# Optimization experiments

Hardware: AMD Instinct MI355X
Metric: run time of the kernel (lower is better)

The kernel has to match this reference:

```python
import jax, jax.numpy as jnp
import numpy as np

B, T, D = 2, 2048, 2048
H, KV = 16, 4
HD = D // H           # head_dim = 128
G = H // KV           # group size = 4
VOCAB = 32000


def setup_inputs() -> dict:
    key = jax.random.key(0)
    k1, k2, k3, k4, k5, k6 = jax.random.split(key, 6)
    hidden_state = jax.random.normal(k1, (B, T, D), dtype=jnp.float32)
    ids = jax.random.randint(k2, (B, T), 1, VOCAB)  # avoid pad id 0
    ids = ids.at[:, T - T // 8:].set(0)             # trailing padding
    inputs_id = ids.astype(jnp.int64)
    s = 1.0 / np.sqrt(D)
    Wq = jax.random.normal(k3, (D, H * HD), dtype=jnp.float32) * s
    Wk = jax.random.normal(k4, (D, KV * HD), dtype=jnp.float32) * s
    Wv = jax.random.normal(k5, (D, KV * HD), dtype=jnp.float32) * s
    Wo = jax.random.normal(k6, (H * HD, D), dtype=jnp.float32) * s
    return {"hidden_state": hidden_state, "inputs_id": inputs_id,
            "Wq": Wq, "Wk": Wk, "Wv": Wv, "Wo": Wo}


def reference(hidden_state, inputs_id, Wq, Wk, Wv, Wo):
    b, t = inputs_id.shape
    # masks: padding over KEYS, combined with causal
    pad = (inputs_id != 0)[:, None, None, :]                 # [B,1,1,T]
    causal = jnp.tril(jnp.ones((t, t), dtype=bool))[None, None]  # [1,1,T,T]
    mask = pad & causal                                       # [B,1,T,T]

    q = (hidden_state @ Wq).reshape(b, t, H, HD).transpose(0, 2, 1, 3)  # [B,H,T,hd]
    k = (hidden_state @ Wk).reshape(b, t, KV, HD)
    v = (hidden_state @ Wv).reshape(b, t, KV, HD)
    # faithful to torch expand/reshape: head h -> kv head (h % KV)
    k = jnp.broadcast_to(k[:, :, None], (b, t, G, KV, HD)).reshape(b, t, H, HD).transpose(0, 2, 1, 3)
    v = jnp.broadcast_to(v[:, :, None], (b, t, G, KV, HD)).reshape(b, t, H, HD).transpose(0, 2, 1, 3)

    scores = jnp.einsum('bhqd,bhkd->bhqk', q, k) / np.sqrt(HD)
    scores = jnp.where(mask, scores, -jnp.inf)
    probs = jax.nn.softmax(scores, axis=-1)
    out = jnp.einsum('bhqk,bhkd->bhqd', probs, v)             # [B,H,T,hd]
    out = out.transpose(0, 2, 1, 3).reshape(b, t, H * HD)
    return out @ Wo
```

## Files before the change

kernel.cpp:

```cpp
#include <hip/hip_runtime.h>

#define B_ 2
#define T_ 2048
#define D_ 2048
#define H_ 16
#define KV_ 4
#define HD_ 128
#define M_ (B_*T_)

typedef __attribute__((ext_vector_type(8))) short s8v;
typedef __attribute__((ext_vector_type(4))) float f4v;
typedef __attribute__((ext_vector_type(16))) float f16v;
typedef __attribute__((ext_vector_type(8))) __bf16 b8v;
typedef __attribute__((ext_vector_type(4))) unsigned u4v;

__device__ __forceinline__ short f2bs(float f) {
  unsigned u = __builtin_bit_cast(unsigned, f);
  u += 0x7fffu + ((u >> 16) & 1u);
  return (short)(u >> 16);
}
__device__ __forceinline__ void plswap2(unsigned &x, unsigned &y) {
  asm volatile("v_permlane32_swap_b32 %0, %1" : "+v"(x), "+v"(y));
}
__device__ __forceinline__ unsigned cvtpk(float lo, float hi) {
  unsigned r;
  asm("v_cvt_pk_bf16_f32 %0, %1, %2" : "=v"(r) : "v"(lo), "v"(hi));
  return r;
}

__global__ void cast_bf16_kernel(const float* __restrict__ in, short* __restrict__ out, int n4) {
  int i = blockIdx.x * 256 + threadIdx.x;
  if (i >= n4) return;
  float4 v = reinterpret_cast<const float4*>(in)[i];
  short4 o;
  o.x = f2bs(v.x); o.y = f2bs(v.y); o.z = f2bs(v.z); o.w = f2bs(v.w);
  reinterpret_cast<short4*>(out)[i] = o;
}

__global__ void tcast_all_kernel(const float* __restrict__ Wq, const float* __restrict__ Wk,
                                 const float* __restrict__ Wv, const float* __restrict__ Wo,
                                 short* __restrict__ WT, short* __restrict__ WoT) {
  __shared__ float t[32][33];
  int bid = blockIdx.x;
  const float* W; short* dst; int N, rowoff;
  if (bid < 4096)      { W = Wq; dst = WT;  N = 2048; rowoff = 0;    }
  else if (bid < 5120) { W = Wk; dst = WT;  N = 512;  rowoff = 2048; bid -= 4096; }
  else if (bid < 6144) { W = Wv; dst = WT;  N = 512;  rowoff = 2560; bid -= 5120; }
  else                 { W = Wo; dst = WoT; N = 2048; rowoff = 0;    bid -= 6144; }
  const int nbl = N >> 5;
  const int nb = (bid % nbl) * 32, kb = (bid / nbl) * 32;
  const int tx = threadIdx.x, ty = threadIdx.y;
#pragma unroll
  for (int j = 0; j < 4; ++j)
    t[ty + j*8][tx] = W[(size_t)(kb + ty + j*8) * N + nb + tx];
  __syncthreads();
#pragma unroll
  for (int j = 0; j < 4; ++j)
    dst[(size_t)(rowoff + nb + ty + j*8) * 2048 + kb + tx] = f2bs(t[tx][ty + j*8]);
}

template<int MODE>
__global__ __launch_bounds__(256) void gemm_bt_kernel(const short* __restrict__ A,
                                                      const short* __restrict__ BT,
                                                      void* __restrict__ Cv,
                                                      short* __restrict__ Kv,
                                                      short* __restrict__ Vt,
                                                      int M, int N, int K) {
  __shared__ alignas(16) short As[2][128*32];
  __shared__ alignas(16) short Bs[2][128*32];
  const int tid  = threadIdx.x;
  const int wave = tid >> 6;
  const int lane = tid & 63;
  const int lr = lane & 15;
  const int lk = (lane >> 4) * 8;
  const int m0 = blockIdx.y * 128;
  const int n0 = blockIdx.x * 128;
  const int wr = (wave >> 1) * 64;
  const int wc = (wave & 1) * 64;

  const int srow = tid >> 2, skc = tid & 3;
  const short* gaBase = A  + (size_t)(m0 + srow) * K + skc*8;
  const short* gbBase = BT + (size_t)(n0 + srow) * K + skc*8;
  const short* gaBase2 = A  + (size_t)(m0 + 64 + srow) * K + skc*8;
  const short* gbBase2 = BT + (size_t)(n0 + 64 + srow) * K + skc*8;
  const int ldsOff  = (wave*64) * 8;
  const int ldsOff2 = (256 + wave*64) * 8;

  f4v acc[4][4];
#pragma unroll
  for (int m = 0; m < 4; ++m)
#pragma unroll
    for (int n = 0; n < 4; ++n) acc[m][n] = (f4v)0.0f;

  {
    __builtin_amdgcn_global_load_lds((const __attribute__((address_space(1))) void*)gaBase,
        (__attribute__((address_space(3))) void*)(&As[0][0] + ldsOff), 16, 0, 0);
    __builtin_amdgcn_global_load_lds((const __attribute__((address_space(1))) void*)gbBase,
        (__attribute__((address_space(3))) void*)(&Bs[0][0] + ldsOff), 16, 0, 0);
    __builtin_amdgcn_global_load_lds((const __attribute__((address_space(1))) void*)gaBase2,
        (__attribute__((address_space(3))) void*)(&As[0][0] + ldsOff2), 16, 0, 0);
    __builtin_amdgcn_global_load_lds((const __attribute__((address_space(1))) void*)gbBase2,
        (__attribute__((address_space(3))) void*)(&Bs[0][0] + ldsOff2), 16, 0, 0);
  }

  int cur = 0;
  for (int k0 = 0; k0 < K; k0 += 32) {
    __syncthreads();
    if (k0 + 32 < K) {
      const int kn = k0 + 32;
      short* a1 = &As[cur^1][0];
      short* b1 = &Bs[cur^1][0];
      __builtin_amdgcn_global_load_lds((const __attribute__((address_space(1))) void*)(gaBase + kn),
          (__attribute__((address_space(3))) void*)(a1 + ldsOff), 16, 0, 0);
      __builtin_amdgcn_global_load_lds((const __attribute__((address_space(1))) void*)(gbBase + kn),
          (__attribute__((address_space(3))) void*)(b1 + ldsOff), 16, 0, 0);
      __builtin_amdgcn_global_load_lds((const __attribute__((address_space(1))) void*)(gaBase2 + kn),
          (__attribute__((address_space(3))) void*)(a1 + ldsOff2), 16, 0, 0);
      __builtin_amdgcn_global_load_lds((const __attribute__((address_space(1))) void*)(gbBase2 + kn),
          (__attribute__((address_space(3))) void*)(b1 + ldsOff2), 16, 0, 0);
    }
    const short* Ac = &As[cur][0];
    const short* Bc = &Bs[cur][0];
    s8v af[4], bfv[4];
#pragma unroll
    for (int m = 0; m < 4; ++m)
      af[m] = *reinterpret_cast<const s8v*>(Ac + (wr + m*16 + lr)*32 + lk);
#pragma unroll
    for (int n = 0; n < 4; ++n)
      bfv[n] = *reinterpret_cast<const s8v*>(Bc + (wc + n*16 + lr)*32 + lk);
#pragma unroll
    for (int m = 0; m < 4; ++m)
#pragma unroll
      for (int n = 0; n < 4; ++n)
        acc[m][n] = __builtin_amdgcn_mfma_f32_16x16x32_bf16(
            __builtin_bit_cast(b8v, af[m]), __builtin_bit_cast(b8v, bfv[n]),
            acc[m][n], 0, 0, 0);
    cur ^= 1;
  }

  if (MODE == 3 && n0 >= 2560) {
#pragma unroll
    for (int m = 0; m < 4; ++m) {
#pragma unroll
      for (int n = 0; n < 4; ++n) {
        const int col = n0 + wc + n*16 + lr - 2560;
        const int row = m0 + wr + m*16 + (lane >> 4)*4;
        short4 o;
        o.x = f2bs(acc[m][n][0]); o.y = f2bs(acc[m][n][1]);
        o.z = f2bs(acc[m][n][2]); o.w = f2bs(acc[m][n][3]);
        *reinterpret_cast<short4*>(Vt + (size_t)col * M + row) = o;
      }
    }
  } else {
#pragma unroll
    for (int m = 0; m < 4; ++m) {
#pragma unroll
      for (int n = 0; n < 4; ++n) {
#pragma unroll
        for (int i = 0; i < 4; ++i) {
          const int row = m0 + wr + m*16 + (lane >> 4)*4 + i;
          const int col = n0 + wc + n*16 + lr;
          if (MODE == 1)
            reinterpret_cast<float*>(Cv)[(size_t)row * N + col] = acc[m][n][i];
          else if (col < 2048)
            reinterpret_cast<short*>(Cv)[(size_t)row * 2048 + col] = f2bs(acc[m][n][i]);
          else
            Kv[(size_t)row * 512 + (col - 2048)] = f2bs(acc[m][n][i]);
        }
      }
    }
  }
}

__device__ __forceinline__ void stage_tile(short* KsBuf, short* VtBuf,
                                           const short* __restrict__ Kb,
                                           const short* __restrict__ Vtg,
                                           int bT, int kv0, int kvh,
                                           int tid, int wave) {
#pragma unroll
  for (int j = 0; j < 4; ++j) {
    const int f = j*256 + tid;
    const int row = f >> 4, cd = f & 15, cs = cd ^ (row & 7);
    const short* g = Kb + (size_t)(bT + kv0 + row)*512 + kvh*HD_ + cs*8;
    short* l = KsBuf + (j*256 + wave*64) * 8;
    __builtin_amdgcn_global_load_lds((const __attribute__((address_space(1))) void*)g,
                                     (__attribute__((address_space(3))) void*)l, 16, 0, 0);
  }
#pragma unroll
  for (int j = 0; j < 4; ++j) {
    const int f = j*256 + tid;
    const int d = f >> 3, cd = f & 7, cs = cd ^ (d & 7);
    const short* g = Vtg + (size_t)(kvh*HD_ + d)*M_ + bT + kv0 + cs*8;
    short* l = VtBuf + (j*256 + wave*64) * 8;
    __builtin_amdgcn_global_load_lds((const __attribute__((address_space(1))) void*)g,
                                     (__attribute__((address_space(3))) void*)l, 16, 0, 0);
  }
}

__global__ __launch_bounds__(256, 2) void attn_kernel(const short* __restrict__ Q,
                                                      const short* __restrict__ Kb,
                                                      const short* __restrict__ Vtg,
                                                      const int* __restrict__ ids,
                                                      short* __restrict__ AO) {
  __shared__ alignas(16) short Ks[2][64*128];
  __shared__ alignas(16) short Vt[2][128*64];

  const int bid = blockIdx.x;
  const int g   = bid & 31;
  const int gr  = bid >> 5;
  const int p   = (gr < 8) ? (15 - gr) : (gr - 8);
  const int h   = g & (H_-1);
  const int b   = g >> 4;
  const int kvh = h & (KV_-1);
  const int tid = threadIdx.x;
  const int wq  = tid >> 6;
  const int lane = tid & 63;
  const int ql  = lane & 31;
  const int hi  = lane >> 5;
  const int bT  = b * T_;
  const int q0  = p * 128;
  const int qrow = q0 + wq*32 + ql;
  const int nt  = 2*(p+1);
  const float SC = 0.08838834764831845f * 1.4426950408889634f;

  s8v qf[8];
  const size_t qgbase = (size_t)(bT + qrow) * (H_*HD_) + h*HD_;
#pragma unroll
  for (int mm = 0; mm < 8; ++mm)
    qf[mm] = *reinterpret_cast<const s8v*>(Q + qgbase + mm*16 + hi*8);

  f16v oacc[4];
#pragma unroll
  for (int n = 0; n < 4; ++n) oacc[n] = (f16v)0.0f;
  float m_run = -1.0e30f, lsum = 0.0f;

  stage_tile(Ks[0], Vt[0], Kb, Vtg, bT, 0, kvh, tid, wq);
  int cur = 0;
  for (int t = 0; t < nt; ++t) {
    __syncthreads();
    if (t + 1 < nt)
      stage_tile(Ks[cur^1], Vt[cur^1], Kb, Vtg, bT, (t+1)*64, kvh, tid, wq);
    const int kv0 = t * 64;
    const char* KsC = reinterpret_cast<const char*>(Ks[cur]);
    const char* VtC = reinterpret_cast<const char*>(Vt[cur]);

    const unsigned long long pmask = __ballot(ids[bT + kv0 + lane] != 0);

    f16v sacc[2];
    sacc[0] = (f16v)0.0f; sacc[1] = (f16v)0.0f;
#pragma unroll
    for (int mm = 0; mm < 8; ++mm) {
#pragma unroll
      for (int kb = 0; kb < 2; ++kb) {
        const int row = kb*32 + ql;
        s8v kf = *reinterpret_cast<const s8v*>(KsC +
            ((row*256 + mm*32 + hi*16) ^ ((row & 7) << 4)));
        sacc[kb] = __builtin_amdgcn_mfma_f32_32x32x16_bf16(
            __builtin_bit_cast(b8v, kf), __builtin_bit_cast(b8v, qf[mm]), sacc[kb], 0, 0, 0);
      }
    }

    float tm[16];
#pragma unroll
    for (int r = 0; r < 16; ++r) tm[r] = fmaxf(sacc[0][r], sacc[1][r]);
#pragma unroll
    for (int r = 0; r < 8; ++r) tm[r] = fmaxf(tm[r], tm[r+8]);
#pragma unroll
    for (int r = 0; r < 4; ++r) tm[r] = fmaxf(tm[r], tm[r+4]);
    tm[0] = fmaxf(fmaxf(tm[0], tm[1]), fmaxf(tm[2], tm[3]));
    const float mx = fmaxf(tm[0], __shfl_xor(tm[0], 32));

    if (!__all(mx <= m_run + 20.0f)) {
      const float mn = fmaxf(m_run, mx);
      const float corr = exp2f((m_run - mn) * SC);
      lsum *= corr;
#pragma unroll
      for (int n = 0; n < 4; ++n)
#pragma unroll
        for (int r = 0; r < 16; ++r) oacc[n][r] *= corr;
      m_run = mn;
    }
    const float nm = -m_run * SC;
    const bool fast = (kv0 + 63 <= q0 + wq*32) && (pmask == ~0ull);

    float psum = 0.0f;
#pragma unroll
    for (int kb = 0; kb < 2; ++kb) {
      float pv[16];
#pragma unroll
      for (int r = 0; r < 16; ++r)
        pv[r] = exp2f(fmaf(sacc[kb][r], SC, nm));
      if (!fast) {
        const int th = qrow - kv0 - kb*32 - 4*hi;
        const unsigned cw = (th >= 28) ? 0xffffffffu
                          : ((th < 0) ? 0u : ((2u << th) - 1u));
        const unsigned vm = cw & (unsigned)(pmask >> (kb*32 + 4*hi));
#pragma unroll
        for (int r = 0; r < 16; ++r) {
          const int C = (r & 3) + 8*(r >> 2);
          pv[r] = ((vm >> C) & 1u) ? pv[r] : 0.0f;
        }
      }
      float ps[8];
#pragma unroll
      for (int r = 0; r < 8; ++r) ps[r] = pv[r] + pv[r+8];
#pragma unroll
      for (int r = 0; r < 4; ++r) ps[r] += ps[r+4];
      psum += (ps[0] + ps[1]) + (ps[2] + ps[3]);

      unsigned pa = cvtpk(pv[0],  pv[1]),  pb = cvtpk(pv[2],  pv[3]);
      unsigned pc = cvtpk(pv[4],  pv[5]),  pd = cvtpk(pv[6],  pv[7]);
      unsigned pe = cvtpk(pv[8],  pv[9]),  pf_ = cvtpk(pv[10], pv[11]);
      unsigned pg = cvtpk(pv[12], pv[13]), ph = cvtpk(pv[14], pv[15]);
      plswap2(pa, pc);  plswap2(pb, pd);
      plswap2(pe, pg);  plswap2(pf_, ph);
      u4v pw0 = {pa, pb, pc, pd};
      u4v pw1 = {pe, pf_, pg, ph};

#pragma unroll
      for (int s = 0; s < 2; ++s) {
        const b8v pf = __builtin_bit_cast(b8v, s ? pw1 : pw0);
        const int ks = 2*kb + s;
#pragma unroll
        for (int n = 0; n < 4; ++n) {
          const int d = n*32 + ql;
          s8v vf = *reinterpret_cast<const s8v*>(VtC +
              ((d*128 + ks*32 + hi*16) ^ ((d & 7) << 4)));
          oacc[n] = __builtin_amdgcn_mfma_f32_32x32x16_bf16(
              __builtin_bit_cast(b8v, vf), pf, oacc[n], 0, 0, 0);
        }
      }
    }
    lsum += psum + __shfl_xor(psum, 32);
    cur ^= 1;
  }

  const float inv = 1.0f / fmaxf(lsum, 1.0e-37f);
  const size_t obase = (size_t)(bT + qrow) * (H_*HD_) + h*HD_;
#pragma unroll
  for (int n = 0; n < 4; ++n) {
#pragma unroll
    for (int j = 0; j < 4; ++j) {
      short4 o;
      o.x = f2bs(oacc[n][4*j+0] * inv);
      o.y = f2bs(oacc[n][4*j+1] * inv);
      o.z = f2bs(oacc[n][4*j+2] * inv);
      o.w = f2bs(oacc[n][4*j+3] * inv);
      *reinterpret_cast<short4*>(AO + obase + n*32 + 8*j + 4*hi) = o;
    }
  }
}

extern "C" void kernel_launch(void* const* d_in, const int* in_sizes, int n_in,
                              void* d_out, int out_size, void* d_ws, size_t ws_size,
                              hipStream_t stream) {
  const float* hs = (const float*)d_in[0];
  const int*  ids = (const int*)d_in[1];
  const float* Wq = (const float*)d_in[2];
  const float* Wk = (const float*)d_in[3];
  const float* Wv = (const float*)d_in[4];
  const float* Wo = (const float*)d_in[5];
  char* ws = (char*)d_ws;

  short* hsb = (short*)(ws);
  short* WT  = (short*)(ws + (16u << 20));
  short* WoT = (short*)(ws + (28u << 20));
  short* Qb  = (short*)(ws + (36u << 20));
  short* Kb  = (short*)(ws + (52u << 20));
  short* Vtg = (short*)(ws + (56u << 20));
  short* AO  = hsb;
  float* out = (float*)d_out;

  cast_bf16_kernel<<<dim3((M_*D_/4 + 255)/256), dim3(256), 0, stream>>>(hs, hsb, M_*D_/4);
  tcast_all_kernel<<<dim3(10240), dim3(32, 8), 0, stream>>>(Wq, Wk, Wv, Wo, WT, WoT);

  gemm_bt_kernel<3><<<dim3(3072/128, 4096/128), dim3(256), 0, stream>>>(
      hsb, WT, Qb, Kb, Vtg, 4096, 3072, 2048);

  attn_kernel<<<dim3(512), dim3(256), 0, stream>>>(Qb, Kb, Vtg, ids, AO);

  gemm_bt_kernel<1><<<dim3(2048/128, 4096/128), dim3(256), 0, stream>>>(
      AO, WoT, out, nullptr, nullptr, 4096, 2048, 2048);
}
```

Before: 211.7 us.

## Software-pipeline attention: overlap next-tile QK MFMA with softmax/PV, triple-buffer V

After: 228.3 us. 1.08x slower.

```diff
diff --git a/kernel.cpp b/kernel.cpp
--- a/kernel.cpp
+++ b/kernel.cpp
@@ -28,7 +28,15 @@
   return r;
 }
 
-__global__ void cast_bf16_kernel(const float* __restrict__ in, short* __restrict__ out, int n4) {
+__global__ void cast_bf16_kernel(const float* __restrict__ in, short* __restrict__ out, int n4,
+                                 const int* __restrict__ ids, unsigned long long* __restrict__ pmA) {
+  if (blockIdx.x == 0 && threadIdx.x < 64) {
+    const int bb = threadIdx.x >> 5, tt = threadIdx.x & 31;
+    const int* p = ids + bb*T_ + tt*64;
+    unsigned long long m = 0;
+    for (int k = 0; k < 64; ++k) m |= (unsigned long long)(p[k] != 0) << k;
+    pmA[threadIdx.x] = m;
+  }
   int i = blockIdx.x * 256 + threadIdx.x;
   if (i >= n4) return;
   float4 v = reinterpret_cast<const float4*>(in)[i];
@@ -172,38 +180,149 @@
   }
 }
 
-__device__ __forceinline__ void stage_tile(short* KsBuf, short* VtBuf,
-                                           const short* __restrict__ Kb,
-                                           const short* __restrict__ Vtg,
-                                           int bT, int kv0, int kvh,
-                                           int tid, int wave) {
+__device__ __forceinline__ void stage_K(short* dst, const short* __restrict__ Kb,
+                                        int bT, int kv0, int kvh, int tid, int wave) {
 #pragma unroll
   for (int j = 0; j < 4; ++j) {
     const int f = j*256 + tid;
     const int row = f >> 4, cd = f & 15, cs = cd ^ (row & 7);
     const short* g = Kb + (size_t)(bT + kv0 + row)*512 + kvh*HD_ + cs*8;
-    short* l = KsBuf + (j*256 + wave*64) * 8;
+    short* l = dst + (j*256 + wave*64) * 8;
     __builtin_amdgcn_global_load_lds((const __attribute__((address_space(1))) void*)g,
                                      (__attribute__((address_space(3))) void*)l, 16, 0, 0);
   }
+}
+__device__ __forceinline__ void stage_V(short* dst, const short* __restrict__ Vtg,
+                                        int bT, int kv0, int kvh, int tid, int wave) {
 #pragma unroll
   for (int j = 0; j < 4; ++j) {
     const int f = j*256 + tid;
     const int d = f >> 3, cd = f & 7, cs = cd ^ (d & 7);
     const short* g = Vtg + (size_t)(kvh*HD_ + d)*M_ + bT + kv0 + cs*8;
-    short* l = VtBuf + (j*256 + wave*64) * 8;
+    short* l = dst + (j*256 + wave*64) * 8;
     __builtin_amdgcn_global_load_lds((const __attribute__((address_space(1))) void*)g,
                                      (__attribute__((address_space(3))) void*)l, 16, 0, 0);
   }
+}
+
+__device__ __forceinline__ void qk_mfma(const char* KsC, const s8v (&qf)[8],
+                                        int ql, int hi, f16v (&sacc)[2]) {
+  sacc[0] = (f16v)0.0f; sacc[1] = (f16v)0.0f;
+#pragma unroll
+  for (int mm = 0; mm < 8; ++mm) {
+#pragma unroll
+    for (int kb = 0; kb < 2; ++kb) {
+      const int row = kb*32 + ql;
+      s8v kf = *reinterpret_cast<const s8v*>(KsC +
+          ((row*256 + mm*32 + hi*16) ^ ((row & 7) << 4)));
+      sacc[kb] = __builtin_amdgcn_mfma_f32_32x32x16_bf16(
+          __builtin_bit_cast(b8v, kf), __builtin_bit_cast(b8v, qf[mm]), sacc[kb], 0, 0, 0);
+    }
+  }
+}
+
+__device__ __forceinline__ void attn_iter(
+    int t, int nt, int q0, int wq, int ql, int hi, int qrow, int bT, int kvh, int tid,
+    const s8v (&qf)[8], f16v (&scur)[2], f16v (&snxt)[2],
+    const char* kr, short* kw, const char* vr, short* vw,
+    const short* __restrict__ Kb, const short* __restrict__ Vtg,
+    unsigned long long &pm_cur, const unsigned long long* __restrict__ pmA, int pmBase,
+    f16v (&oacc)[4], float &m_run, float &lsum, float SC)
+{
+  if (t + 1 < nt) { asm volatile("s_waitcnt vmcnt(4)" ::: "memory"); }
+  else            { asm volatile("s_waitcnt vmcnt(0)" ::: "memory"); }
+  __builtin_amdgcn_s_barrier();
+  __builtin_amdgcn_sched_barrier(0);
+
+  if (t + 2 < nt) stage_K(kw, Kb, bT, (t+2)*64, kvh, tid, wq);
+  if (t + 1 < nt) qk_mfma(kr, qf, ql, hi, snxt);
+  unsigned long long pm_next = (t + 1 < nt) ? pmA[pmBase + t + 1] : 0ull;
+
+  const int kv0 = t * 64;
+  float tm[16];
+#pragma unroll
+  for (int r = 0; r < 16; ++r) tm[r] = fmaxf(scur[0][r], scur[1][r]);
+#pragma unroll
+  for (int r = 0; r < 8; ++r) tm[r] = fmaxf(tm[r], tm[r+8]);
+#pragma unroll
+  for (int r = 0; r < 4; ++r) tm[r] = fmaxf(tm[r], tm[r+4]);
+  tm[0] = fmaxf(fmaxf(tm[0], tm[1]), fmaxf(tm[2], tm[3]));
+  const float mx = fmaxf(tm[0], __shfl_xor(tm[0], 32));
+
+  if (!__all(mx <= m_run + 20.0f)) {
+    const float mn = fmaxf(m_run, mx);
+    const float corr = exp2f((m_run - mn) * SC);
+    lsum *= corr;
+#pragma unroll
+    for (int n = 0; n < 4; ++n)
+#pragma unroll
+      for (int r = 0; r < 16; ++r) oacc[n][r] *= corr;
+    m_run = mn;
+  }
+  const float nm = -m_run * SC;
+  const bool fast = (kv0 + 63 <= q0 + wq*32) && (pm_cur == ~0ull);
+
+  float psum = 0.0f;
+#pragma unroll
+  for (int kb = 0; kb < 2; ++kb) {
+    float pv[16];
+#pragma unroll
+    for (int r = 0; r < 16; ++r)
+      pv[r] = exp2f(fmaf(scur[kb][r], SC, nm));
+    if (!fast) {
+      const int th = qrow - kv0 - kb*32 - 4*hi;
+      const unsigned cw = (th >= 28) ? 0xffffffffu
+                        : ((th < 0) ? 0u : ((2u << th) - 1u));
+      const unsigned vm = cw & (unsigned)(pm_cur >> (kb*32 + 4*hi));
+#pragma unroll
+      for (int r = 0; r < 16; ++r) {
+        const int C = (r & 3) + 8*(r >> 2);
+        pv[r] = ((vm >> C) & 1u) ? pv[r] : 0.0f;
+      }
+    }
+    float ps[8];
+#pragma unroll
+    for (int r = 0; r < 8; ++r) ps[r] = pv[r] + pv[r+8];
+#pragma unroll
+    for (int r = 0; r < 4; ++r) ps[r] += ps[r+4];
+    psum += (ps[0] + ps[1]) + (ps[2] + ps[3]);
+
+    unsigned pa = cvtpk(pv[0],  pv[1]),  pb = cvtpk(pv[2],  pv[3]);
+    unsigned pc = cvtpk(pv[4],  pv[5]),  pd = cvtpk(pv[6],  pv[7]);
+    unsigned pe = cvtpk(pv[8],  pv[9]),  pf_ = cvtpk(pv[10], pv[11]);
+    unsigned pg = cvtpk(pv[12], pv[13]), ph = cvtpk(pv[14], pv[15]);
+    plswap2(pa, pc);  plswap2(pb, pd);
+    plswap2(pe, pg);  plswap2(pf_, ph);
+    u4v pw0 = {pa, pb, pc, pd};
+    u4v pw1 = {pe, pf_, pg, ph};
+
+#pragma unroll
+    for (int s = 0; s < 2; ++s) {
+      const b8v pf = __builtin_bit_cast(b8v, s ? pw1 : pw0);
+      const int ks = 2*kb + s;
+#pragma unroll
+      for (int n = 0; n < 4; ++n) {
+        const int d = n*32 + ql;
+        s8v vf = *reinterpret_cast<const s8v*>(vr +
+            ((d*128 + ks*32 + hi*16) ^ ((d & 7) << 4)));
+        oacc[n] = __builtin_amdgcn_mfma_f32_32x32x16_bf16(
+            __builtin_bit_cast(b8v, vf), pf, oacc[n], 0, 0, 0);
+      }
+    }
+  }
+  lsum += psum + __shfl_xor(psum, 32);
+
+  if (t + 2 < nt) stage_V(vw, Vtg, bT, (t+2)*64, kvh, tid, wq);
+  pm_cur = pm_next;
 }
 
 __global__ __launch_bounds__(256, 2) void attn_kernel(const short* __restrict__ Q,
                                                       const short* __restrict__ Kb,
                                                       const short* __restrict__ Vtg,
-                                                      const int* __restrict__ ids,
+                                                      const unsigned long long* __restrict__ pmA,
                                                       short* __restrict__ AO) {
   __shared__ alignas(16) short Ks[2][64*128];
-  __shared__ alignas(16) short Vt[2][128*64];
+  __shared__ alignas(16) short Vs[3][128*64];
 
   const int bid = blockIdx.x;
   const int g   = bid & 31;
@@ -221,6 +340,7 @@
   const int q0  = p * 128;
   const int qrow = q0 + wq*32 + ql;
   const int nt  = 2*(p+1);
+  const int pmBase = b * 32;
   const float SC = 0.08838834764831845f * 1.4426950408889634f;
 
   s8v qf[8];
@@ -234,105 +354,28 @@
   for (int n = 0; n < 4; ++n) oacc[n] = (f16v)0.0f;
   float m_run = -1.0e30f, lsum = 0.0f;
 
-  stage_tile(Ks[0], Vt[0], Kb, Vtg, bT, 0, kvh, tid, wq);
-  int cur = 0;
-  for (int t = 0; t < nt; ++t) {
-    __syncthreads();
-    if (t + 1 < nt)
-      stage_tile(Ks[cur^1], Vt[cur^1], Kb, Vtg, bT, (t+1)*64, kvh, tid, wq);
-    const int kv0 = t * 64;
-    const char* KsC = reinterpret_cast<const char*>(Ks[cur]);
-    const char* VtC = reinterpret_cast<const char*>(Vt[cur]);
-
-    const unsigned long long pmask = __ballot(ids[bT + kv0 + lane] != 0);
-
-    f16v sacc[2];
-    sacc[0] = (f16v)0.0f; sacc[1] = (f16v)0.0f;
-#pragma unroll
-    for (int mm = 0; mm < 8; ++mm) {
-#pragma unroll
-      for (int kb = 0; kb < 2; ++kb) {
-        const int row = kb*32 + ql;
-        s8v kf = *reinterpret_cast<const s8v*>(KsC +
-            ((row*256 + mm*32 + hi*16) ^ ((row & 7) << 4)));
-        sacc[kb] = __builtin_amdgcn_mfma_f32_32x32x16_bf16(
-            __builtin_bit_cast(b8v, kf), __builtin_bit_cast(b8v, qf[mm]), sacc[kb], 0, 0, 0);
-      }
-    }
-
-    float tm[16];
-#pragma unroll
-    for (int r = 0; r < 16; ++r) tm[r] = fmaxf(sacc[0][r], sacc[1][r]);
-#pragma unroll
-    for (int r = 0; r < 8; ++r) tm[r] = fmaxf(tm[r], tm[r+8]);
-#pragma unroll
-    for (int r = 0; r < 4; ++r) tm[r] = fmaxf(tm[r], tm[r+4]);
-    tm[0] = fmaxf(fmaxf(tm[0], tm[1]), fmaxf(tm[2], tm[3]));
-    const float mx = fmaxf(tm[0], __shfl_xor(tm[0], 32));
-
-    if (!__all(mx <= m_run + 20.0f)) {
-      const float mn = fmaxf(m_run, mx);
-      const float corr = exp2f((m_run - mn) * SC);
-      lsum *= corr;
-#pragma unroll
-      for (int n = 0; n < 4; ++n)
-#pragma unroll
-        for (int r = 0; r < 16; ++r) oacc[n][r] *= corr;
-      m_run = mn;
-    }
-    const float nm = -m_run * SC;
-    const bool fast = (kv0 + 63 <= q0 + wq*32) && (pmask == ~0ull);
-
-    float psum = 0.0f;
-#pragma unroll
-    for (int kb = 0; kb < 2; ++kb) {
-      float pv[16];
-#pragma unroll
-      for (int r = 0; r < 16; ++r)
-        pv[r] = exp2f(fmaf(sacc[kb][r], SC, nm));
-      if (!fast) {
-        const int th = qrow - kv0 - kb*32 - 4*hi;
-        const unsigned cw = (th >= 28) ? 0xffffffffu
-                          : ((th < 0) ? 0u : ((2u << th) - 1u));
-        const unsigned vm = cw & (unsigned)(pmask >> (kb*32 + 4*hi));
-#pragma unroll
-        for (int r = 0; r < 16; ++r) {
-          const int C = (r & 3) + 8*(r >> 2);
-          pv[r] = ((vm >> C) & 1u) ? pv[r] : 0.0f;
-        }
-      }
-      float ps[8];
-#pragma unroll
-      for (int r = 0; r < 8; ++r) ps[r] = pv[r] + pv[r+8];
-#pragma unroll
-      for (int r = 0; r < 4; ++r) ps[r] += ps[r+4];
-      psum += (ps[0] + ps[1]) + (ps[2] + ps[3]);
-
-      unsigned pa = cvtpk(pv[0],  pv[1]),  pb = cvtpk(pv[2],  pv[3]);
-      unsigned pc = cvtpk(pv[4],  pv[5]),  pd = cvtpk(pv[6],  pv[7]);
-      unsigned pe = cvtpk(pv[8],  pv[9]),  pf_ = cvtpk(pv[10], pv[11]);
-      unsigned pg = cvtpk(pv[12], pv[13]), ph = cvtpk(pv[14], pv[15]);
-      plswap2(pa, pc);  plswap2(pb, pd);
-      plswap2(pe, pg);  plswap2(pf_, ph);
-      u4v pw0 = {pa, pb, pc, pd};
-      u4v pw1 = {pe, pf_, pg, ph};
-
-#pragma unroll
-      for (int s = 0; s < 2; ++s) {
-        const b8v pf = __builtin_bit_cast(b8v, s ? pw1 : pw0);
-        const int ks = 2*kb + s;
-#pragma unroll
-        for (int n = 0; n < 4; ++n) {
-          const int d = n*32 + ql;
-          s8v vf = *reinterpret_cast<const s8v*>(VtC +
-              ((d*128 + ks*32 + hi*16) ^ ((d & 7) << 4)));
-          oacc[n] = __builtin_amdgcn_mfma_f32_32x32x16_bf16(
-              __builtin_bit_cast(b8v, vf), pf, oacc[n], 0, 0, 0);
-        }
-      }
-    }
-    lsum += psum + __shfl_xor(psum, 32);
-    cur ^= 1;
+  stage_K(Ks[0], Kb, bT, 0,  kvh, tid, wq);
+  stage_V(Vs[0], Vtg, bT, 0,  kvh, tid, wq);
+  stage_K(Ks[1], Kb, bT, 64, kvh, tid, wq);
+  stage_V(Vs[1], Vtg, bT, 64, kvh, tid, wq);
+  unsigned long long pm_cur = pmA[pmBase];
+  asm volatile("s_waitcnt vmcnt(8)" ::: "memory");
+  __builtin_amdgcn_s_barrier();
+  __builtin_amdgcn_sched_barrier(0);
+
+  f16v sE[2], sO[2];
+  qk_mfma((const char*)Ks[0], qf, ql, hi, sE);
+
+  char* v0 = (char*)Vs[0]; char* v1 = (char*)Vs[1]; char* v2 = (char*)Vs[2];
+  for (int t = 0; t < nt; t += 2) {
+    attn_iter(t, nt, q0, wq, ql, hi, qrow, bT, kvh, tid, qf, sE, sO,
+              (const char*)Ks[1], Ks[0], v0, (short*)v2,
+              Kb, Vtg, pm_cur, pmA, pmBase, oacc, m_run, lsum, SC);
+    { char* tmp = v0; v0 = v1; v1 = v2; v2 = tmp; }
+    attn_iter(t+1, nt, q0, wq, ql, hi, qrow, bT, kvh, tid, qf, sO, sE,
+              (const char*)Ks[0], Ks[1], v0, (short*)v2,
+              Kb, Vtg, pm_cur, pmA, pmBase, oacc, m_run, lsum, SC);
+    { char* tmp = v0; v0 = v1; v1 = v2; v2 = tmp; }
   }
 
   const float inv = 1.0f / fmaxf(lsum, 1.0e-37f);
@@ -370,14 +413,15 @@
   short* Vtg = (short*)(ws + (56u << 20));
   short* AO  = hsb;
   float* out = (float*)d_out;
-
-  cast_bf16_kernel<<<dim3((M_*D_/4 + 255)/256), dim3(256), 0, stream>>>(hs, hsb, M_*D_/4);
+  unsigned long long* pmA = (unsigned long long*)d_out;
+
+  cast_bf16_kernel<<<dim3((M_*D_/4 + 255)/256), dim3(256), 0, stream>>>(hs, hsb, M_*D_/4, ids, pmA);
   tcast_all_kernel<<<dim3(10240), dim3(32, 8), 0, stream>>>(Wq, Wk, Wv, Wo, WT, WoT);
 
   gemm_bt_kernel<3><<<dim3(3072/128, 4096/128), dim3(256), 0, stream>>>(
       hsb, WT, Qb, Kb, Vtg, 4096, 3072, 2048);
 
-  attn_kernel<<<dim3(512), dim3(256), 0, stream>>>(Qb, Kb, Vtg, ids, AO);
+  attn_kernel<<<dim3(512), dim3(256), 0, stream>>>(Qb, Kb, Vtg, pmA, AO);
 
   gemm_bt_kernel<1><<<dim3(2048/128, 4096/128), dim3(256), 0, stream>>>(
       AO, WoT, out, nullptr, nullptr, 4096, 2048, 2048);
```

## Triple-buffer GEMM LDS pipeline and merge cast kernels into one prep launch

Applied to the files above, without the earlier changes.

New measurement: 212.6 us. Within noise of the previous version (+0.4%).

```diff
diff --git a/kernel.cpp b/kernel.cpp
--- a/kernel.cpp
+++ b/kernel.cpp
@@ -28,20 +28,22 @@
   return r;
 }
 
-__global__ void cast_bf16_kernel(const float* __restrict__ in, short* __restrict__ out, int n4) {
-  int i = blockIdx.x * 256 + threadIdx.x;
-  if (i >= n4) return;
-  float4 v = reinterpret_cast<const float4*>(in)[i];
-  short4 o;
-  o.x = f2bs(v.x); o.y = f2bs(v.y); o.z = f2bs(v.z); o.w = f2bs(v.w);
-  reinterpret_cast<short4*>(out)[i] = o;
-}
-
-__global__ void tcast_all_kernel(const float* __restrict__ Wq, const float* __restrict__ Wk,
-                                 const float* __restrict__ Wv, const float* __restrict__ Wo,
-                                 short* __restrict__ WT, short* __restrict__ WoT) {
+__global__ void prep_kernel(const float* __restrict__ hs,
+                            const float* __restrict__ Wq, const float* __restrict__ Wk,
+                            const float* __restrict__ Wv, const float* __restrict__ Wo,
+                            short* __restrict__ hsb,
+                            short* __restrict__ WT, short* __restrict__ WoT) {
+  int bid = blockIdx.x;
+  const int tid = threadIdx.y * 32 + threadIdx.x;
+  if (bid >= 10240) {
+    const int i = (bid - 10240) * 256 + tid;
+    float4 v = reinterpret_cast<const float4*>(hs)[i];
+    short4 o;
+    o.x = f2bs(v.x); o.y = f2bs(v.y); o.z = f2bs(v.z); o.w = f2bs(v.w);
+    reinterpret_cast<short4*>(hsb)[i] = o;
+    return;
+  }
   __shared__ float t[32][33];
-  int bid = blockIdx.x;
   const float* W; short* dst; int N, rowoff;
   if (bid < 4096)      { W = Wq; dst = WT;  N = 2048; rowoff = 0;    }
   else if (bid < 5120) { W = Wk; dst = WT;  N = 512;  rowoff = 2048; bid -= 4096; }
@@ -66,8 +68,8 @@
                                                       short* __restrict__ Kv,
                                                       short* __restrict__ Vt,
                                                       int M, int N, int K) {
-  __shared__ alignas(16) short As[2][128*32];
-  __shared__ alignas(16) short Bs[2][128*32];
+  __shared__ alignas(16) short As[3][128*32];
+  __shared__ alignas(16) short Bs[3][128*32];
   const int tid  = threadIdx.x;
   const int wave = tid >> 6;
   const int lane = tid & 63;
@@ -79,8 +81,8 @@
   const int wc = (wave & 1) * 64;
 
   const int srow = tid >> 2, skc = tid & 3;
-  const short* gaBase = A  + (size_t)(m0 + srow) * K + skc*8;
-  const short* gbBase = BT + (size_t)(n0 + srow) * K + skc*8;
+  const short* gaBase  = A  + (size_t)(m0 + srow) * K + skc*8;
+  const short* gbBase  = BT + (size_t)(n0 + srow) * K + skc*8;
   const short* gaBase2 = A  + (size_t)(m0 + 64 + srow) * K + skc*8;
   const short* gbBase2 = BT + (size_t)(n0 + 64 + srow) * K + skc*8;
   const int ldsOff  = (wave*64) * 8;
@@ -92,35 +94,31 @@
 #pragma unroll
     for (int n = 0; n < 4; ++n) acc[m][n] = (f4v)0.0f;
 
-  {
-    __builtin_amdgcn_global_load_lds((const __attribute__((address_space(1))) void*)gaBase,
-        (__attribute__((address_space(3))) void*)(&As[0][0] + ldsOff), 16, 0, 0);
-    __builtin_amdgcn_global_load_lds((const __attribute__((address_space(1))) void*)gbBase,
-        (__attribute__((address_space(3))) void*)(&Bs[0][0] + ldsOff), 16, 0, 0);
-    __builtin_amdgcn_global_load_lds((const __attribute__((address_space(1))) void*)gaBase2,
-        (__attribute__((address_space(3))) void*)(&As[0][0] + ldsOff2), 16, 0, 0);
-    __builtin_amdgcn_global_load_lds((const __attribute__((address_space(1))) void*)gbBase2,
-        (__attribute__((address_space(3))) void*)(&Bs[0][0] + ldsOff2), 16, 0, 0);
-  }
-
-  int cur = 0;
-  for (int k0 = 0; k0 < K; k0 += 32) {
-    __syncthreads();
-    if (k0 + 32 < K) {
-      const int kn = k0 + 32;
-      short* a1 = &As[cur^1][0];
-      short* b1 = &Bs[cur^1][0];
-      __builtin_amdgcn_global_load_lds((const __attribute__((address_space(1))) void*)(gaBase + kn),
-          (__attribute__((address_space(3))) void*)(a1 + ldsOff), 16, 0, 0);
-      __builtin_amdgcn_global_load_lds((const __attribute__((address_space(1))) void*)(gbBase + kn),
-          (__attribute__((address_space(3))) void*)(b1 + ldsOff), 16, 0, 0);
-      __builtin_amdgcn_global_load_lds((const __attribute__((address_space(1))) void*)(gaBase2 + kn),
-          (__attribute__((address_space(3))) void*)(a1 + ldsOff2), 16, 0, 0);
-      __builtin_amdgcn_global_load_lds((const __attribute__((address_space(1))) void*)(gbBase2 + kn),
-          (__attribute__((address_space(3))) void*)(b1 + ldsOff2), 16, 0, 0);
-    }
-    const short* Ac = &As[cur][0];
-    const short* Bc = &Bs[cur][0];
+  auto STAGE = [&](int tile, int slot) {
+    const int kn = tile * 32;
+    short* a1 = &As[slot][0];
+    short* b1 = &Bs[slot][0];
+    __builtin_amdgcn_global_load_lds((const __attribute__((address_space(1))) void*)(gaBase + kn),
+        (__attribute__((address_space(3))) void*)(a1 + ldsOff), 16, 0, 0);
+    __builtin_amdgcn_global_load_lds((const __attribute__((address_space(1))) void*)(gbBase + kn),
+        (__attribute__((address_space(3))) void*)(b1 + ldsOff), 16, 0, 0);
+    __builtin_amdgcn_global_load_lds((const __attribute__((address_space(1))) void*)(gaBase2 + kn),
+        (__attribute__((address_space(3))) void*)(a1 + ldsOff2), 16, 0, 0);
+    __builtin_amdgcn_global_load_lds((const __attribute__((address_space(1))) void*)(gbBase2 + kn),
+        (__attribute__((address_space(3))) void*)(b1 + ldsOff2), 16, 0, 0);
+  };
+
+  const int NT = K >> 5;
+  STAGE(0, 0);
+  STAGE(1, 1);
+  asm volatile("s_waitcnt vmcnt(4)" ::: "memory");
+  __builtin_amdgcn_s_barrier();
+  __builtin_amdgcn_sched_barrier(0);
+
+  for (int t = 0; t < NT; ++t) {
+    if (t + 2 < NT) STAGE(t + 2, (t + 2) % 3);
+    const short* Ac = &As[t % 3][0];
+    const short* Bc = &Bs[t % 3][0];
     s8v af[4], bfv[4];
 #pragma unroll
     for (int m = 0; m < 4; ++m)
@@ -135,7 +133,12 @@
         acc[m][n] = __builtin_amdgcn_mfma_f32_16x16x32_bf16(
             __builtin_bit_cast(b8v, af[m]), __builtin_bit_cast(b8v, bfv[n]),
             acc[m][n], 0, 0, 0);
-    cur ^= 1;
+    if (t + 1 < NT) {
+      if (t < NT - 2) { asm volatile("s_waitcnt vmcnt(4)" ::: "memory"); }
+      else            { asm volatile("s_waitcnt vmcnt(0)" ::: "memory"); }
+      __builtin_amdgcn_s_barrier();
+      __builtin_amdgcn_sched_barrier(0);
+    }
   }
 
   if (MODE == 3 && n0 >= 2560) {
@@ -371,8 +374,7 @@
   short* AO  = hsb;
   float* out = (float*)d_out;
 
-  cast_bf16_kernel<<<dim3((M_*D_/4 + 255)/256), dim3(256), 0, stream>>>(hs, hsb, M_*D_/4);
-  tcast_all_kernel<<<dim3(10240), dim3(32, 8), 0, stream>>>(Wq, Wk, Wv, Wo, WT, WoT);
+  prep_kernel<<<dim3(18432), dim3(32, 8), 0, stream>>>(hs, Wq, Wk, Wv, Wo, hsb, WT, WoT);
 
   gemm_bt_kernel<3><<<dim3(3072/128, 4096/128), dim3(256), 0, stream>>>(
       hsb, WT, Qb, Kb, Vtg, 4096, 3072, 2048);
```
